# Kernel optimization log

Hardware: AMD Instinct MI355X
Metric: run time of the kernel (lower is better)

The kernel has to match this reference:

```python
import jax, jax.numpy as jnp
import numpy as np

MAX_LEN = 200
MAX_K = 3
ITERATION = 3
NEG_PAD = -2.0 ** 16 + 1.0


def setup_inputs() -> dict:
    key = jax.random.key(0)
    k1, k2, k3, k4 = jax.random.split(key, 4)
    B, L, D_in, D_out = 1024, MAX_LEN, 128, 128
    low_capsule = jax.random.normal(k1, (B, L, D_in), dtype=jnp.float32)
    B_matrix = jax.random.normal(k2, (1, MAX_K, L), dtype=jnp.float32)
    S_matrix = jax.random.normal(k3, (D_in, D_out), dtype=jnp.float32)
    # lengths in [1, MAX_LEN]; at least one row hits MAX_LEN so max(seq_len)==MAX_LEN
    seq_len = jax.random.randint(k4, (B, 1), 1, MAX_LEN + 1, dtype=jnp.int64)
    seq_len = seq_len.at[0, 0].set(MAX_LEN)
    return {"low_capsule": low_capsule, "B_matrix": B_matrix,
            "S_matrix": S_matrix, "seq_len": seq_len}


def squash(x):
    # torch code: norm over dim=1 (the capsule axis), keepdim
    sq = jnp.sum(jnp.square(x), axis=1, keepdims=True)
    scale = sq / (1.0 + sq) / jnp.sqrt(sq + 1e-9)
    return scale * x


def reference(low_capsule, B_matrix, S_matrix, seq_len):
    # low_capsule: [B, L, D_in], B_matrix: [1, K, L], S_matrix: [D_in, D_out], seq_len: [B, 1]
    # mask: [B, K, L] (seq_len tiled over K via broadcasting)
    mask = jnp.arange(MAX_LEN)[None, None, :] < seq_len[:, :, None]
    # bilinear projection is loop-invariant (same math as recomputing each iter)
    low_new = jnp.einsum('bld,de->ble', low_capsule, S_matrix)  # [B, L, D_out]
    high = None
    for _ in range(ITERATION):
        logits = jnp.where(mask, B_matrix, jnp.float32(NEG_PAD))  # [B, K, L]
        W = jax.nn.softmax(logits, axis=-1)
        high = squash(jnp.einsum('bkl,ble->bke', W, low_new))  # [B, K, D_out]
        # agreement, summed over batch with keepdim -> [1, K, L]
        B_delta = jnp.einsum('bke,ble->kl', high, low_new)[None]
        B_matrix = B_matrix + B_delta
    return high
```

## Files before the change

kernel.cpp:

```cpp
#include <hip/hip_runtime.h>
#include <math.h>

#define BATCH 1024
#define SEQ   200
#define DIN   128
#define DOUT  128
#define PSTR  608

__global__ __launch_bounds__(256) void k_transpose(const float* __restrict__ S,
                                                   float* __restrict__ ST) {
    int idx = blockIdx.x * 256 + threadIdx.x;
    int d = idx >> 7, e = idx & 127;
    ST[e * DIN + d] = S[d * DOUT + e];
}

__global__ __launch_bounds__(256, 2) void k_iter(
    const float* __restrict__ A,
    const float* __restrict__ S,
    const float* __restrict__ ST,
    const float* __restrict__ Bm,
    const int* __restrict__ seq,
    const float* __restrict__ acc0, const float* __restrict__ acc1,
    float* __restrict__ part,
    float* __restrict__ out, int iter) {
    __shared__ float sW[SEQ * 4];
    __shared__ float pB[4][3][DIN];
    __shared__ float sWA[3][DIN];
    __shared__ float sH[3][DIN];
    __shared__ float sHS[3][DIN];

    const int t = threadIdx.x;
    const int lane = t & 63, w = t >> 6;
    const int b = blockIdx.x;
    const float* Ab = A + (size_t)b * (SEQ * DIN);
    const int n = seq[b];

    if (w < 3) {
        const int k = w;
        float v0[4], v1[4], v2[4];
#pragma unroll
        for (int i = 0; i < 4; ++i) {
            int l = lane + 64 * i;
            bool inb = (l < SEQ);
            v0[i] = inb ? Bm[k * SEQ + l] : 0.f;
            v1[i] = (inb && iter >= 1) ? acc0[k * SEQ + l] : 0.f;
            v2[i] = (inb && iter >= 2) ? acc1[k * SEQ + l] : 0.f;
        }
        float vv[4], m = -INFINITY;
#pragma unroll
        for (int i = 0; i < 4; ++i) {
            int l = lane + 64 * i;
            float v = v0[i] + v1[i] + v2[i];
            vv[i] = (l < n) ? v : -INFINITY;
            if (l < n) m = fmaxf(m, v);
        }
        for (int off = 32; off; off >>= 1) m = fmaxf(m, __shfl_xor(m, off, 64));
        float s = 0.f, pv[4];
#pragma unroll
        for (int i = 0; i < 4; ++i) {
            pv[i] = (vv[i] == -INFINITY) ? 0.f : expf(vv[i] - m);
            s += pv[i];
        }
        for (int off = 32; off; off >>= 1) s += __shfl_xor(s, off, 64);
        float rs = 1.f / s;
#pragma unroll
        for (int i = 0; i < 4; ++i) {
            int l = lane + 64 * i;
            if (l < SEQ) sW[l * 4 + k] = pv[i] * rs;
        }
    }
    __syncthreads();

    {
        const float2* a2 = (const float2*)Ab;
        float h00 = 0.f, h01 = 0.f, h10 = 0.f, h11 = 0.f, h20 = 0.f, h21 = 0.f;
        const int l0 = w * 50;

#define PB_FMA(WV, V) \
        h00 = fmaf(WV.x, V.x, h00); h01 = fmaf(WV.x, V.y, h01); \
        h10 = fmaf(WV.y, V.x, h10); h11 = fmaf(WV.y, V.y, h11); \
        h20 = fmaf(WV.z, V.x, h20); h21 = fmaf(WV.z, V.y, h21);

        for (int g = 0; g < 6; ++g) {
            const int lb = l0 + g * 8;
            float2 v0 = a2[(size_t)(lb + 0) * 64 + lane];
            float2 v1 = a2[(size_t)(lb + 1) * 64 + lane];
            float2 v2 = a2[(size_t)(lb + 2) * 64 + lane];
            float2 v3 = a2[(size_t)(lb + 3) * 64 + lane];
            float2 v4 = a2[(size_t)(lb + 4) * 64 + lane];
            float2 v5 = a2[(size_t)(lb + 5) * 64 + lane];
            float2 v6 = a2[(size_t)(lb + 6) * 64 + lane];
            float2 v7 = a2[(size_t)(lb + 7) * 64 + lane];
            float4 w0 = *(const float4*)&sW[(lb + 0) * 4];
            float4 w1 = *(const float4*)&sW[(lb + 1) * 4];
            float4 w2 = *(const float4*)&sW[(lb + 2) * 4];
            float4 w3 = *(const float4*)&sW[(lb + 3) * 4];
            float4 w4 = *(const float4*)&sW[(lb + 4) * 4];
            float4 w5 = *(const float4*)&sW[(lb + 5) * 4];
            float4 w6 = *(const float4*)&sW[(lb + 6) * 4];
            float4 w7 = *(const float4*)&sW[(lb + 7) * 4];
            PB_FMA(w0, v0) PB_FMA(w1, v1) PB_FMA(w2, v2) PB_FMA(w3, v3)
            PB_FMA(w4, v4) PB_FMA(w5, v5) PB_FMA(w6, v6) PB_FMA(w7, v7)
        }
        {
            const int lb = l0 + 48;
            float2 v0 = a2[(size_t)(lb + 0) * 64 + lane];
            float2 v1 = a2[(size_t)(lb + 1) * 64 + lane];
            float4 w0 = *(const float4*)&sW[(lb + 0) * 4];
            float4 w1 = *(const float4*)&sW[(lb + 1) * 4];
            PB_FMA(w0, v0) PB_FMA(w1, v1)
        }
#undef PB_FMA
        pB[w][0][2 * lane] = h00; pB[w][0][2 * lane + 1] = h01;
        pB[w][1][2 * lane] = h10; pB[w][1][2 * lane + 1] = h11;
        pB[w][2][2 * lane] = h20; pB[w][2][2 * lane + 1] = h21;
    }
    __syncthreads();

    if (t < DIN) {
#pragma unroll
        for (int k = 0; k < 3; ++k)
            sWA[k][t] = pB[0][k][t] + pB[1][k][t] + pB[2][k][t] + pB[3][k][t];
    }
    __syncthreads();

    {
        const int e = t & 127, hh = t >> 7;
        const float* Scol = S + e;
        float g0 = 0.f, g1 = 0.f, g2 = 0.f;
        for (int g = 0; g < 8; ++g) {
            const int db = hh * 64 + g * 8;
            float s0 = Scol[(db + 0) * DOUT];
            float s1 = Scol[(db + 1) * DOUT];
            float s2 = Scol[(db + 2) * DOUT];
            float s3 = Scol[(db + 3) * DOUT];
            float s4 = Scol[(db + 4) * DOUT];
            float s5 = Scol[(db + 5) * DOUT];
            float s6 = Scol[(db + 6) * DOUT];
            float s7 = Scol[(db + 7) * DOUT];
#define HB_FMA(J, SV) \
            g0 = fmaf(sWA[0][db + J], SV, g0); \
            g1 = fmaf(sWA[1][db + J], SV, g1); \
            g2 = fmaf(sWA[2][db + J], SV, g2);
            HB_FMA(0, s0) HB_FMA(1, s1) HB_FMA(2, s2) HB_FMA(3, s3)
            HB_FMA(4, s4) HB_FMA(5, s5) HB_FMA(6, s6) HB_FMA(7, s7)
#undef HB_FMA
        }
        pB[hh][0][e] = g0; pB[hh][1][e] = g1; pB[hh][2][e] = g2;
    }
    __syncthreads();

    if (t < DIN) {
        float g0 = pB[0][0][t] + pB[1][0][t];
        float g1 = pB[0][1][t] + pB[1][1][t];
        float g2 = pB[0][2][t] + pB[1][2][t];
        float sq = g0 * g0 + g1 * g1 + g2 * g2;
        float scale = sq / (1.f + sq) / sqrtf(sq + 1e-9f);
        g0 *= scale; g1 *= scale; g2 *= scale;
        if (iter == 2) {
            size_t o = (size_t)b * 3 * DOUT + t;
            out[o] = g0; out[o + DOUT] = g1; out[o + 2 * DOUT] = g2;
        } else {
            sH[0][t] = g0; sH[1][t] = g1; sH[2][t] = g2;
        }
    }
    if (iter == 2) return;
    __syncthreads();

    {
        const int d = t & 127, hh = t >> 7;
        const float* STcol = ST + d;
        float s0a = 0.f, s1a = 0.f, s2a = 0.f;
        for (int g = 0; g < 8; ++g) {
            const int eb = hh * 64 + g * 8;
            float s0 = STcol[(eb + 0) * DIN];
            float s1 = STcol[(eb + 1) * DIN];
            float s2 = STcol[(eb + 2) * DIN];
            float s3 = STcol[(eb + 3) * DIN];
            float s4 = STcol[(eb + 4) * DIN];
            float s5 = STcol[(eb + 5) * DIN];
            float s6 = STcol[(eb + 6) * DIN];
            float s7 = STcol[(eb + 7) * DIN];
#define HS_FMA(J, SV) \
            s0a = fmaf(sH[0][eb + J], SV, s0a); \
            s1a = fmaf(sH[1][eb + J], SV, s1a); \
            s2a = fmaf(sH[2][eb + J], SV, s2a);
            HS_FMA(0, s0) HS_FMA(1, s1) HS_FMA(2, s2) HS_FMA(3, s3)
            HS_FMA(4, s4) HS_FMA(5, s5) HS_FMA(6, s6) HS_FMA(7, s7)
#undef HS_FMA
        }
        pB[hh][0][d] = s0a; pB[hh][1][d] = s1a; pB[hh][2][d] = s2a;
    }
    __syncthreads();

    if (t < DIN) {
#pragma unroll
        for (int k = 0; k < 3; ++k)
            sHS[k][t] = pB[0][k][t] + pB[1][k][t];
    }
    __syncthreads();

    if (t < SEQ) {
        const float* row = Ab + (size_t)t * DIN;
        float d0 = 0.f, d1 = 0.f, d2 = 0.f;
        for (int g = 0; g < 4; ++g) {
            const int jb = g * 8;
            float4 u0 = *(const float4*)&row[4 * (jb + 0)];
            float4 u1 = *(const float4*)&row[4 * (jb + 1)];
            float4 u2 = *(const float4*)&row[4 * (jb + 2)];
            float4 u3 = *(const float4*)&row[4 * (jb + 3)];
            float4 u4 = *(const float4*)&row[4 * (jb + 4)];
            float4 u5 = *(const float4*)&row[4 * (jb + 5)];
            float4 u6 = *(const float4*)&row[4 * (jb + 6)];
            float4 u7 = *(const float4*)&row[4 * (jb + 7)];
#define PC_FMA(J, U) { \
            float4 x0 = *(const float4*)&sHS[0][4 * (jb + J)]; \
            float4 x1 = *(const float4*)&sHS[1][4 * (jb + J)]; \
            float4 x2 = *(const float4*)&sHS[2][4 * (jb + J)]; \
            d0 += x0.x * U.x + x0.y * U.y + x0.z * U.z + x0.w * U.w; \
            d1 += x1.x * U.x + x1.y * U.y + x1.z * U.z + x1.w * U.w; \
            d2 += x2.x * U.x + x2.y * U.y + x2.z * U.z + x2.w * U.w; }
            PC_FMA(0, u0) PC_FMA(1, u1) PC_FMA(2, u2) PC_FMA(3, u3)
            PC_FMA(4, u4) PC_FMA(5, u5) PC_FMA(6, u6) PC_FMA(7, u7)
#undef PC_FMA
        }
        float* pp = part + (size_t)b * PSTR;
        pp[t] = d0;
        pp[SEQ + t] = d1;
        pp[2 * SEQ + t] = d2;
    }
}

__global__ __launch_bounds__(256) void k_reduce(const float* __restrict__ part,
                                                float* __restrict__ accN) {
    __shared__ float sP[4][4];
    const int t = threadIdx.x, lane = t & 63, w = t >> 6;
    const int c4 = blockIdx.x * 4;
    float4 v0 = *(const float4*)&part[(size_t)(t + 256 * 0) * PSTR + c4];
    float4 v1 = *(const float4*)&part[(size_t)(t + 256 * 1) * PSTR + c4];
    float4 v2 = *(const float4*)&part[(size_t)(t + 256 * 2) * PSTR + c4];
    float4 v3 = *(const float4*)&part[(size_t)(t + 256 * 3) * PSTR + c4];
    float sx = v0.x + v1.x + v2.x + v3.x;
    float sy = v0.y + v1.y + v2.y + v3.y;
    float sz = v0.z + v1.z + v2.z + v3.z;
    float sw = v0.w + v1.w + v2.w + v3.w;
#pragma unroll
    for (int off = 1; off < 64; off <<= 1) {
        sx += __shfl_xor(sx, off, 64);
        sy += __shfl_xor(sy, off, 64);
        sz += __shfl_xor(sz, off, 64);
        sw += __shfl_xor(sw, off, 64);
    }
    if (lane == 0) { sP[w][0] = sx; sP[w][1] = sy; sP[w][2] = sz; sP[w][3] = sw; }
    __syncthreads();
    if (t < 4)
        accN[c4 + t] = sP[0][t] + sP[1][t] + sP[2][t] + sP[3][t];
}

extern "C" void kernel_launch(void* const* d_in, const int* in_sizes, int n_in,
                              void* d_out, int out_size, void* d_ws, size_t ws_size,
                              hipStream_t stream) {
    const float* low_capsule = (const float*)d_in[0];
    const float* B_matrix    = (const float*)d_in[1];
    const float* S_matrix    = (const float*)d_in[2];
    const int*   seq_len     = (const int*)d_in[3];
    float* out = (float*)d_out;

    float* ST   = (float*)d_ws;
    float* acc0 = ST + 16384;
    float* acc1 = acc0 + 640;
    float* part = acc1 + 640;

    k_transpose<<<64, 256, 0, stream>>>(S_matrix, ST);

    k_iter<<<BATCH, 256, 0, stream>>>(low_capsule, S_matrix, ST, B_matrix,
                                      seq_len, acc0, acc1, part, out, 0);
    k_reduce<<<150, 256, 0, stream>>>(part, acc0);
    k_iter<<<BATCH, 256, 0, stream>>>(low_capsule, S_matrix, ST, B_matrix,
                                      seq_len, acc0, acc1, part, out, 1);
    k_reduce<<<150, 256, 0, stream>>>(part, acc1);
    k_iter<<<BATCH, 256, 0, stream>>>(low_capsule, S_matrix, ST, B_matrix,
                                      seq_len, acc0, acc1, part, out, 2);
}
```

Baseline: 250.0 us.

## Split fused routing iteration into scan, weighted-sum, projection, and agreement kernels

Replaces the monolithic per-batch iteration kernel with separate kernels. A tiny prefix-scan kernel precomputes the softmax max and inverse sum for every possible sequence length. A weighted-sum kernel split over two blocks per batch recomputes the softmax weights inline. A projection/squash kernel and a separate agreement kernel follow. The aim is more parallelism and occupancy in the memory-bound passes over the input, but it adds launches and global round-trips for the intermediates. The serial O(L) scan per thread in the 3-block scan kernel adds a latency step to each iteration.

```diff
diff --git a/kernel.cpp b/kernel.cpp
--- a/kernel.cpp
+++ b/kernel.cpp
@@ -14,113 +14,106 @@
     ST[e * DIN + d] = S[d * DOUT + e];
 }
 
-__global__ __launch_bounds__(256, 2) void k_iter(
-    const float* __restrict__ A,
-    const float* __restrict__ S,
-    const float* __restrict__ ST,
-    const float* __restrict__ Bm,
-    const int* __restrict__ seq,
-    const float* __restrict__ acc0, const float* __restrict__ acc1,
-    float* __restrict__ part,
-    float* __restrict__ out, int iter) {
-    __shared__ float sW[SEQ * 4];
+__global__ __launch_bounds__(256) void k_scan(const float* __restrict__ Bm,
+                                              const float* __restrict__ a0,
+                                              const float* __restrict__ a1,
+                                              float* __restrict__ v,
+                                              float* __restrict__ Mn,
+                                              float* __restrict__ iEn, int iter) {
+    __shared__ float sv[SEQ];
+    const int k = blockIdx.x, t = threadIdx.x;
+    if (t < SEQ) {
+        float x = Bm[k * SEQ + t];
+        if (iter >= 1) x += a0[k * SEQ + t];
+        if (iter >= 2) x += a1[k * SEQ + t];
+        sv[t] = x;
+        v[k * SEQ + t] = x;
+    }
+    __syncthreads();
+    if (t < SEQ) {
+        const int n = t + 1;
+        float m = -INFINITY, s = 0.f;
+        for (int l = 0; l < n; ++l) {
+            float x = sv[l];
+            float nm = fmaxf(m, x);
+            s = s * expf(m - nm) + expf(x - nm);
+            m = nm;
+        }
+        Mn[k * 201 + n] = m;
+        iEn[k * 201 + n] = 1.f / s;
+    }
+}
+
+__global__ __launch_bounds__(256, 4) void k_wa(const float* __restrict__ A,
+                                               const float* __restrict__ v,
+                                               const float* __restrict__ Mn,
+                                               const float* __restrict__ iEn,
+                                               const int* __restrict__ seq,
+                                               float* __restrict__ pw) {
     __shared__ float pB[4][3][DIN];
+    const int t = threadIdx.x, lane = t & 63, w = t >> 6;
+    const int b = blockIdx.x >> 1, half = blockIdx.x & 1;
+    const int n = seq[b];
+    const float2* a2 = (const float2*)(A + (size_t)b * (SEQ * DIN));
+    const float M0 = Mn[n],       E0 = iEn[n];
+    const float M1 = Mn[201 + n], E1 = iEn[201 + n];
+    const float M2 = Mn[402 + n], E2 = iEn[402 + n];
+    const int l0 = half * 100 + w * 25;
+    float h00 = 0.f, h01 = 0.f, h10 = 0.f, h11 = 0.f, h20 = 0.f, h21 = 0.f;
+
+#define WROW(L, V) { \
+    float w0 = ((L) < n) ? expf(v[(L)] - M0) * E0 : 0.f;       \
+    float w1 = ((L) < n) ? expf(v[200 + (L)] - M1) * E1 : 0.f; \
+    float w2 = ((L) < n) ? expf(v[400 + (L)] - M2) * E2 : 0.f; \
+    h00 = fmaf(w0, (V).x, h00); h01 = fmaf(w0, (V).y, h01);    \
+    h10 = fmaf(w1, (V).x, h10); h11 = fmaf(w1, (V).y, h11);    \
+    h20 = fmaf(w2, (V).x, h20); h21 = fmaf(w2, (V).y, h21); }
+
+    for (int g = 0; g < 3; ++g) {
+        const int lb = l0 + g * 8;
+        float2 v0 = a2[(size_t)(lb + 0) * 64 + lane];
+        float2 v1 = a2[(size_t)(lb + 1) * 64 + lane];
+        float2 v2 = a2[(size_t)(lb + 2) * 64 + lane];
+        float2 v3 = a2[(size_t)(lb + 3) * 64 + lane];
+        float2 v4 = a2[(size_t)(lb + 4) * 64 + lane];
+        float2 v5 = a2[(size_t)(lb + 5) * 64 + lane];
+        float2 v6 = a2[(size_t)(lb + 6) * 64 + lane];
+        float2 v7 = a2[(size_t)(lb + 7) * 64 + lane];
+        WROW(lb + 0, v0) WROW(lb + 1, v1) WROW(lb + 2, v2) WROW(lb + 3, v3)
+        WROW(lb + 4, v4) WROW(lb + 5, v5) WROW(lb + 6, v6) WROW(lb + 7, v7)
+    }
+    {
+        float2 v0 = a2[(size_t)(l0 + 24) * 64 + lane];
+        WROW(l0 + 24, v0)
+    }
+#undef WROW
+
+    pB[w][0][2 * lane] = h00; pB[w][0][2 * lane + 1] = h01;
+    pB[w][1][2 * lane] = h10; pB[w][1][2 * lane + 1] = h11;
+    pB[w][2][2 * lane] = h20; pB[w][2][2 * lane + 1] = h21;
+    __syncthreads();
+    if (t < DIN) {
+        float* dst = pw + ((size_t)b * 2 + half) * 384;
+        dst[t]       = pB[0][0][t] + pB[1][0][t] + pB[2][0][t] + pB[3][0][t];
+        dst[128 + t] = pB[0][1][t] + pB[1][1][t] + pB[2][1][t] + pB[3][1][t];
+        dst[256 + t] = pB[0][2][t] + pB[1][2][t] + pB[2][2][t] + pB[3][2][t];
+    }
+}
+
+__global__ __launch_bounds__(256) void k_mid(const float* __restrict__ pw,
+                                             const float* __restrict__ S,
+                                             const float* __restrict__ ST,
+                                             float* __restrict__ hs,
+                                             float* __restrict__ out, int iter) {
     __shared__ float sWA[3][DIN];
+    __shared__ float pb2[2][3][DIN];
     __shared__ float sH[3][DIN];
-    __shared__ float sHS[3][DIN];
-
-    const int t = threadIdx.x;
-    const int lane = t & 63, w = t >> 6;
-    const int b = blockIdx.x;
-    const float* Ab = A + (size_t)b * (SEQ * DIN);
-    const int n = seq[b];
-
-    if (w < 3) {
-        const int k = w;
-        float v0[4], v1[4], v2[4];
-#pragma unroll
-        for (int i = 0; i < 4; ++i) {
-            int l = lane + 64 * i;
-            bool inb = (l < SEQ);
-            v0[i] = inb ? Bm[k * SEQ + l] : 0.f;
-            v1[i] = (inb && iter >= 1) ? acc0[k * SEQ + l] : 0.f;
-            v2[i] = (inb && iter >= 2) ? acc1[k * SEQ + l] : 0.f;
-        }
-        float vv[4], m = -INFINITY;
-#pragma unroll
-        for (int i = 0; i < 4; ++i) {
-            int l = lane + 64 * i;
-            float v = v0[i] + v1[i] + v2[i];
-            vv[i] = (l < n) ? v : -INFINITY;
-            if (l < n) m = fmaxf(m, v);
-        }
-        for (int off = 32; off; off >>= 1) m = fmaxf(m, __shfl_xor(m, off, 64));
-        float s = 0.f, pv[4];
-#pragma unroll
-        for (int i = 0; i < 4; ++i) {
-            pv[i] = (vv[i] == -INFINITY) ? 0.f : expf(vv[i] - m);
-            s += pv[i];
-        }
-        for (int off = 32; off; off >>= 1) s += __shfl_xor(s, off, 64);
-        float rs = 1.f / s;
-#pragma unroll
-        for (int i = 0; i < 4; ++i) {
-            int l = lane + 64 * i;
-            if (l < SEQ) sW[l * 4 + k] = pv[i] * rs;
-        }
-    }
-    __syncthreads();
-
-    {
-        const float2* a2 = (const float2*)Ab;
-        float h00 = 0.f, h01 = 0.f, h10 = 0.f, h11 = 0.f, h20 = 0.f, h21 = 0.f;
-        const int l0 = w * 50;
-
-#define PB_FMA(WV, V) \
-        h00 = fmaf(WV.x, V.x, h00); h01 = fmaf(WV.x, V.y, h01); \
-        h10 = fmaf(WV.y, V.x, h10); h11 = fmaf(WV.y, V.y, h11); \
-        h20 = fmaf(WV.z, V.x, h20); h21 = fmaf(WV.z, V.y, h21);
-
-        for (int g = 0; g < 6; ++g) {
-            const int lb = l0 + g * 8;
-            float2 v0 = a2[(size_t)(lb + 0) * 64 + lane];
-            float2 v1 = a2[(size_t)(lb + 1) * 64 + lane];
-            float2 v2 = a2[(size_t)(lb + 2) * 64 + lane];
-            float2 v3 = a2[(size_t)(lb + 3) * 64 + lane];
-            float2 v4 = a2[(size_t)(lb + 4) * 64 + lane];
-            float2 v5 = a2[(size_t)(lb + 5) * 64 + lane];
-            float2 v6 = a2[(size_t)(lb + 6) * 64 + lane];
-            float2 v7 = a2[(size_t)(lb + 7) * 64 + lane];
-            float4 w0 = *(const float4*)&sW[(lb + 0) * 4];
-            float4 w1 = *(const float4*)&sW[(lb + 1) * 4];
-            float4 w2 = *(const float4*)&sW[(lb + 2) * 4];
-            float4 w3 = *(const float4*)&sW[(lb + 3) * 4];
-            float4 w4 = *(const float4*)&sW[(lb + 4) * 4];
-            float4 w5 = *(const float4*)&sW[(lb + 5) * 4];
-            float4 w6 = *(const float4*)&sW[(lb + 6) * 4];
-            float4 w7 = *(const float4*)&sW[(lb + 7) * 4];
-            PB_FMA(w0, v0) PB_FMA(w1, v1) PB_FMA(w2, v2) PB_FMA(w3, v3)
-            PB_FMA(w4, v4) PB_FMA(w5, v5) PB_FMA(w6, v6) PB_FMA(w7, v7)
-        }
-        {
-            const int lb = l0 + 48;
-            float2 v0 = a2[(size_t)(lb + 0) * 64 + lane];
-            float2 v1 = a2[(size_t)(lb + 1) * 64 + lane];
-            float4 w0 = *(const float4*)&sW[(lb + 0) * 4];
-            float4 w1 = *(const float4*)&sW[(lb + 1) * 4];
-            PB_FMA(w0, v0) PB_FMA(w1, v1)
-        }
-#undef PB_FMA
-        pB[w][0][2 * lane] = h00; pB[w][0][2 * lane + 1] = h01;
-        pB[w][1][2 * lane] = h10; pB[w][1][2 * lane + 1] = h11;
-        pB[w][2][2 * lane] = h20; pB[w][2][2 * lane + 1] = h21;
-    }
-    __syncthreads();
-
-    if (t < DIN) {
-#pragma unroll
-        for (int k = 0; k < 3; ++k)
-            sWA[k][t] = pB[0][k][t] + pB[1][k][t] + pB[2][k][t] + pB[3][k][t];
+    const int t = threadIdx.x, b = blockIdx.x;
+    const float* p0 = pw + (size_t)b * 2 * 384;
+    if (t < DIN) {
+        sWA[0][t] = p0[t]       + p0[384 + t];
+        sWA[1][t] = p0[128 + t] + p0[384 + 128 + t];
+        sWA[2][t] = p0[256 + t] + p0[384 + 256 + t];
     }
     __syncthreads();
 
@@ -146,14 +139,14 @@
             HB_FMA(4, s4) HB_FMA(5, s5) HB_FMA(6, s6) HB_FMA(7, s7)
 #undef HB_FMA
         }
-        pB[hh][0][e] = g0; pB[hh][1][e] = g1; pB[hh][2][e] = g2;
-    }
-    __syncthreads();
-
-    if (t < DIN) {
-        float g0 = pB[0][0][t] + pB[1][0][t];
-        float g1 = pB[0][1][t] + pB[1][1][t];
-        float g2 = pB[0][2][t] + pB[1][2][t];
+        pb2[hh][0][e] = g0; pb2[hh][1][e] = g1; pb2[hh][2][e] = g2;
+    }
+    __syncthreads();
+
+    if (t < DIN) {
+        float g0 = pb2[0][0][t] + pb2[1][0][t];
+        float g1 = pb2[0][1][t] + pb2[1][1][t];
+        float g2 = pb2[0][2][t] + pb2[1][2][t];
         float sq = g0 * g0 + g1 * g1 + g2 * g2;
         float scale = sq / (1.f + sq) / sqrtf(sq + 1e-9f);
         g0 *= scale; g1 *= scale; g2 *= scale;
@@ -189,46 +182,50 @@
             HS_FMA(4, s4) HS_FMA(5, s5) HS_FMA(6, s6) HS_FMA(7, s7)
 #undef HS_FMA
         }
-        pB[hh][0][d] = s0a; pB[hh][1][d] = s1a; pB[hh][2][d] = s2a;
-    }
-    __syncthreads();
-
-    if (t < DIN) {
-#pragma unroll
-        for (int k = 0; k < 3; ++k)
-            sHS[k][t] = pB[0][k][t] + pB[1][k][t];
-    }
-    __syncthreads();
-
-    if (t < SEQ) {
-        const float* row = Ab + (size_t)t * DIN;
-        float d0 = 0.f, d1 = 0.f, d2 = 0.f;
-        for (int g = 0; g < 4; ++g) {
-            const int jb = g * 8;
-            float4 u0 = *(const float4*)&row[4 * (jb + 0)];
-            float4 u1 = *(const float4*)&row[4 * (jb + 1)];
-            float4 u2 = *(const float4*)&row[4 * (jb + 2)];
-            float4 u3 = *(const float4*)&row[4 * (jb + 3)];
-            float4 u4 = *(const float4*)&row[4 * (jb + 4)];
-            float4 u5 = *(const float4*)&row[4 * (jb + 5)];
-            float4 u6 = *(const float4*)&row[4 * (jb + 6)];
-            float4 u7 = *(const float4*)&row[4 * (jb + 7)];
+        pb2[hh][0][d] = s0a; pb2[hh][1][d] = s1a; pb2[hh][2][d] = s2a;
+    }
+    __syncthreads();
+    if (t < DIN) {
+        float* dst = hs + (size_t)b * 384;
+        dst[t]       = pb2[0][0][t] + pb2[1][0][t];
+        dst[128 + t] = pb2[0][1][t] + pb2[1][1][t];
+        dst[256 + t] = pb2[0][2][t] + pb2[1][2][t];
+    }
+}
+
+__global__ __launch_bounds__(256, 2) void k_pc(const float* __restrict__ A,
+                                               const float* __restrict__ hs,
+                                               float* __restrict__ part) {
+    const int t = threadIdx.x, b = blockIdx.x;
+    if (t >= SEQ) return;
+    const float* row = A + (size_t)b * (SEQ * DIN) + (size_t)t * DIN;
+    const float* h = hs + (size_t)b * 384;
+    float d0 = 0.f, d1 = 0.f, d2 = 0.f;
+    for (int g = 0; g < 4; ++g) {
+        const int jb = g * 8;
+        float4 u0 = *(const float4*)&row[4 * (jb + 0)];
+        float4 u1 = *(const float4*)&row[4 * (jb + 1)];
+        float4 u2 = *(const float4*)&row[4 * (jb + 2)];
+        float4 u3 = *(const float4*)&row[4 * (jb + 3)];
+        float4 u4 = *(const float4*)&row[4 * (jb + 4)];
+        float4 u5 = *(const float4*)&row[4 * (jb + 5)];
+        float4 u6 = *(const float4*)&row[4 * (jb + 6)];
+        float4 u7 = *(const float4*)&row[4 * (jb + 7)];
 #define PC_FMA(J, U) { \
-            float4 x0 = *(const float4*)&sHS[0][4 * (jb + J)]; \
-            float4 x1 = *(const float4*)&sHS[1][4 * (jb + J)]; \
-            float4 x2 = *(const float4*)&sHS[2][4 * (jb + J)]; \
-            d0 += x0.x * U.x + x0.y * U.y + x0.z * U.z + x0.w * U.w; \
-            d1 += x1.x * U.x + x1.y * U.y + x1.z * U.z + x1.w * U.w; \
-            d2 += x2.x * U.x + x2.y * U.y + x2.z * U.z + x2.w * U.w; }
-            PC_FMA(0, u0) PC_FMA(1, u1) PC_FMA(2, u2) PC_FMA(3, u3)
-            PC_FMA(4, u4) PC_FMA(5, u5) PC_FMA(6, u6) PC_FMA(7, u7)
+        float4 x0 = *(const float4*)&h[4 * (jb + J)];       \
+        float4 x1 = *(const float4*)&h[128 + 4 * (jb + J)]; \
+        float4 x2 = *(const float4*)&h[256 + 4 * (jb + J)]; \
+        d0 += x0.x * U.x + x0.y * U.y + x0.z * U.z + x0.w * U.w; \
+        d1 += x1.x * U.x + x1.y * U.y + x1.z * U.z + x1.w * U.w; \
+        d2 += x2.x * U.x + x2.y * U.y + x2.z * U.z + x2.w * U.w; }
+        PC_FMA(0, u0) PC_FMA(1, u1) PC_FMA(2, u2) PC_FMA(3, u3)
+        PC_FMA(4, u4) PC_FMA(5, u5) PC_FMA(6, u6) PC_FMA(7, u7)
 #undef PC_FMA
-        }
-        float* pp = part + (size_t)b * PSTR;
-        pp[t] = d0;
-        pp[SEQ + t] = d1;
-        pp[2 * SEQ + t] = d2;
-    }
+    }
+    float* pp = part + (size_t)b * PSTR;
+    pp[t] = d0;
+    pp[SEQ + t] = d1;
+    pp[2 * SEQ + t] = d2;
 }
 
 __global__ __launch_bounds__(256) void k_reduce(const float* __restrict__ part,
@@ -267,18 +264,30 @@
     float* out = (float*)d_out;
 
     float* ST   = (float*)d_ws;
-    float* acc0 = ST + 16384;
+    float* vL   = ST + 16384;
+    float* Mn   = vL + 640;
+    float* iEn  = Mn + 640;
+    float* acc0 = iEn + 640;
     float* acc1 = acc0 + 640;
-    float* part = acc1 + 640;
+    float* pw   = acc1 + 640;
+    float* hsg  = pw + 786432;
+    float* part = hsg + 393216;
 
     k_transpose<<<64, 256, 0, stream>>>(S_matrix, ST);
 
-    k_iter<<<BATCH, 256, 0, stream>>>(low_capsule, S_matrix, ST, B_matrix,
-                                      seq_len, acc0, acc1, part, out, 0);
+    k_scan<<<3, 256, 0, stream>>>(B_matrix, acc0, acc1, vL, Mn, iEn, 0);
+    k_wa<<<2 * BATCH, 256, 0, stream>>>(low_capsule, vL, Mn, iEn, seq_len, pw);
+    k_mid<<<BATCH, 256, 0, stream>>>(pw, S_matrix, ST, hsg, out, 0);
+    k_pc<<<BATCH, 256, 0, stream>>>(low_capsule, hsg, part);
     k_reduce<<<150, 256, 0, stream>>>(part, acc0);
-    k_iter<<<BATCH, 256, 0, stream>>>(low_capsule, S_matrix, ST, B_matrix,
-                                      seq_len, acc0, acc1, part, out, 1);
+
+    k_scan<<<3, 256, 0, stream>>>(B_matrix, acc0, acc1, vL, Mn, iEn, 1);
+    k_wa<<<2 * BATCH, 256, 0, stream>>>(low_capsule, vL, Mn, iEn, seq_len, pw);
+    k_mid<<<BATCH, 256, 0, stream>>>(pw, S_matrix, ST, hsg, out, 1);
+    k_pc<<<BATCH, 256, 0, stream>>>(low_capsule, hsg, part);
     k_reduce<<<150, 256, 0, stream>>>(part, acc1);
-    k_iter<<<BATCH, 256, 0, stream>>>(low_capsule, S_matrix, ST, B_matrix,
-                                      seq_len, acc0, acc1, part, out, 2);
-}
+
+    k_scan<<<3, 256, 0, stream>>>(B_matrix, acc0, acc1, vL, Mn, iEn, 2);
+    k_wa<<<2 * BATCH, 256, 0, stream>>>(low_capsule, vL, Mn, iEn, seq_len, pw);
+    k_mid<<<BATCH, 256, 0, stream>>>(pw, S_matrix, ST, hsg, out, 2);
+}
```

Measured after the change: 560.4 us. +124.2%, slower.
